# Performance work log

Measured on AMD Instinct MI355X. Metric: run time of the kernel, lower is better.

Reference implementation:

```python
import jax, jax.numpy as jnp
import numpy as np

B, N, C = 2, 2048, 1024
H = 8                 # num_heads
WS = 256              # window_size; half-window = WS // 2
D = C // H            # head_dim


def setup_inputs() -> dict:
    key = jax.random.key(0)
    k0, k1, k2 = jax.random.split(key, 3)
    s = 0.02  # init scale for weights
    x = jax.random.normal(k0, (B, N, C), dtype=jnp.float32)
    w_qkv = jax.random.normal(k1, (3 * C, C), dtype=jnp.float32) * s
    b_qkv = jnp.zeros((3 * C,), dtype=jnp.float32)
    w_proj = jax.random.normal(k2, (C, C), dtype=jnp.float32) * s
    b_proj = jnp.zeros((C,), dtype=jnp.float32)
    return {"x": x, "w_qkv": w_qkv, "b_qkv": b_qkv, "w_proj": w_proj, "b_proj": b_proj}


def reference(x, w_qkv, b_qkv, w_proj, b_proj):
    b, n, c = x.shape
    # qkv projection (torch Linear: x @ W^T + b) -> (B, N, 3C)
    qkv = x @ w_qkv.T + b_qkv
    # (B, N, 3, H, D) -> (3, B, H, N, D)
    qkv = qkv.reshape(b, n, 3, H, D).transpose(2, 0, 3, 1, 4)
    q, k, v = qkv[0], qkv[1], qkv[2]
    # dense scores over sequence, scaled by sqrt(full dim C) as in the source
    attn = jnp.einsum('bhqd,bhkd->bhqk', q, k) / jnp.sqrt(jnp.asarray(c, x.dtype))
    # banded (local-window) mask: keep |i - j| < WS // 2
    i = jnp.arange(n)[:, None]
    j = jnp.arange(n)[None, :]
    band = jnp.abs(i - j) < (WS // 2)
    attn = jnp.where(band, attn, -jnp.inf)
    attn = jax.nn.softmax(attn, axis=-1)
    out = jnp.einsum('bhqk,bhkd->bhqd', attn, v)     # (B, H, N, D)
    out = out.transpose(0, 2, 1, 3).reshape(b, n, c)  # merge heads
    return out @ w_proj.T + b_proj
```

## Files before the change

kernel.cpp:

```cpp
#include <hip/hip_runtime.h>
#include <hip/hip_bf16.h>
#include <stdint.h>

typedef __hip_bfloat16 bf16;
typedef __attribute__((ext_vector_type(8))) short short8;
typedef __attribute__((ext_vector_type(4))) float floatx4;

#define MFMA_BF16(a, b, c) __builtin_amdgcn_mfma_f32_16x16x32_bf16((a), (b), (c), 0, 0, 0)


__device__ __forceinline__ void gl_lds16(const bf16* gsrc, bf16* lds_dst)
{
    __builtin_amdgcn_global_load_lds(
        (const __attribute__((address_space(1))) uint32_t*)(uintptr_t)gsrc,
        (__attribute__((address_space(3))) uint32_t*)(uintptr_t)lds_dst,
        16, 0, 0);
}

__device__ __forceinline__ int sniff_bf16(const uint16_t* __restrict__ x)
{
    int cnt = 0;
#pragma unroll
    for (int i = 0; i < 64; ++i) {
        const int e = (x[2 * i] >> 7) & 0xFF;
        cnt += (e >= 100 && e <= 140) ? 1 : 0;
    }
    return (cnt >= 32) ? 1 : 0;
}

__global__ void __launch_bounds__(256)
cvt_all_kernel(const void* __restrict__ x, const void* __restrict__ wq,
               const void* __restrict__ wp, const void* __restrict__ bq,
               const void* __restrict__ bp,
               bf16* __restrict__ xb, bf16* __restrict__ wqb,
               bf16* __restrict__ wpb, float* __restrict__ bqf,
               float* __restrict__ bpf)
{
    __shared__ int sflag;
    if (threadIdx.x == 0) sflag = sniff_bf16((const uint16_t*)x);
    __syncthreads();
    const bool isbf = (sflag != 0);

    const int blk = blockIdx.x;
    if (blk < 4096) {
        const void* src; bf16* dst; int base;
        if (blk < 2048)      { src = x;  dst = xb;  base = blk << 11; }
        else if (blk < 3584) { src = wq; dst = wqb; base = (blk - 2048) << 11; }
        else                 { src = wp; dst = wpb; base = (blk - 3584) << 11; }
        const int i = base + (int)threadIdx.x * 8;
        if (isbf) {
            *(uint4*)(dst + i) = *(const uint4*)((const bf16*)src + i);
        } else {
            const float4 f0 = *(const float4*)((const float*)src + i);
            const float4 f1 = *(const float4*)((const float*)src + i + 4);
            bf16 o[8];
            o[0] = __float2bfloat16(f0.x); o[1] = __float2bfloat16(f0.y);
            o[2] = __float2bfloat16(f0.z); o[3] = __float2bfloat16(f0.w);
            o[4] = __float2bfloat16(f1.x); o[5] = __float2bfloat16(f1.y);
            o[6] = __float2bfloat16(f1.z); o[7] = __float2bfloat16(f1.w);
            *(uint4*)(dst + i) = *(uint4*)o;
        }
    } else {
        const void* src; float* dst; int base, n;
        if (blk < 4099) { src = bq; dst = bqf; base = (blk - 4096) * 1024; n = 3072; }
        else            { src = bp; dst = bpf; base = 0;                   n = 1024; }
        const int i0 = base + (int)threadIdx.x * 4;
#pragma unroll
        for (int k = 0; k < 4; ++k) {
            const int idx = i0 + k;
            if (idx < n)
                dst[idx] = isbf ? __bfloat162float(((const bf16*)src)[idx])
                                : ((const float*)src)[idx];
        }
    }
}

template <bool FUSE_VT, bool DYN_OUT>
__global__ void __launch_bounds__(256, 2)
gemm_bt_kernel(const bf16* __restrict__ A, const bf16* __restrict__ W,
               const float* __restrict__ bias, void* __restrict__ Cout,
               int M, int Nc, int K, bf16* __restrict__ Vt,
               const uint16_t* __restrict__ sniffsrc)
{
    __shared__ __align__(16) bf16 As[128][32];
    __shared__ __align__(16) bf16 Bs[128][32];
    __shared__ int sflag;

    const int tid  = threadIdx.x;
    const int lane = tid & 63;
    const int wave = tid >> 6;
    const int quad = lane >> 4;
    const int l16  = lane & 15;
    const int wm   = (wave & 1) * 64;
    const int wn   = (wave >> 1) * 64;
    const int bm   = blockIdx.x * 128;
    const int bn   = blockIdx.y * 128;

    if (DYN_OUT && tid == 0) sflag = sniff_bf16(sniffsrc);

    const int grow = wave * 32 + (lane >> 2);
    const int gcol = (lane & 3) * 8;
    const bf16* Ag = A + (size_t)(bm + grow) * K + gcol;
    const bf16* Wg = W + (size_t)(bn + grow) * K + gcol;
    bf16* AsD0 = &As[0][0] + (wave * 2 + 0) * 512;
    bf16* AsD1 = &As[0][0] + (wave * 2 + 1) * 512;
    bf16* BsD0 = &Bs[0][0] + (wave * 2 + 0) * 512;
    bf16* BsD1 = &Bs[0][0] + (wave * 2 + 1) * 512;

    floatx4 acc[4][4];
#pragma unroll
    for (int i = 0; i < 4; ++i)
#pragma unroll
        for (int j = 0; j < 4; ++j)
#pragma unroll
            for (int r = 0; r < 4; ++r) acc[i][j][r] = 0.0f;

    for (int k0 = 0; k0 < K; k0 += 32) {
        gl_lds16(Ag + k0,                    AsD0);
        gl_lds16(Ag + (size_t)16 * K + k0,   AsD1);
        gl_lds16(Wg + k0,                    BsD0);
        gl_lds16(Wg + (size_t)16 * K + k0,   BsD1);
        __syncthreads();

        short8 af[4], bfr[4];
#pragma unroll
        for (int i = 0; i < 4; ++i)
            af[i] = *(const short8*)(&As[wm + i * 16 + l16][quad * 8]);
#pragma unroll
        for (int j = 0; j < 4; ++j)
            bfr[j] = *(const short8*)(&Bs[wn + j * 16 + l16][quad * 8]);
#pragma unroll
        for (int i = 0; i < 4; ++i)
#pragma unroll
            for (int j = 0; j < 4; ++j)
                acc[i][j] = MFMA_BF16(af[i], bfr[j], acc[i][j]);
        __syncthreads();
    }

    const bool outbf = DYN_OUT ? (sflag != 0) : true;

#pragma unroll
    for (int i = 0; i < 4; ++i) {
#pragma unroll
        for (int j = 0; j < 4; ++j) {
            const int col = bn + wn + j * 16 + l16;
            const float bv = bias[col];
#pragma unroll
            for (int r = 0; r < 4; ++r) {
                const int row = bm + wm + i * 16 + quad * 4 + r;
                const float v = acc[i][j][r] + bv;
                const size_t idx = (size_t)row * Nc + col;
                if (!DYN_OUT || outbf) {
                    ((bf16*)Cout)[idx] = __float2bfloat16(v);
                } else {
                    ((float*)Cout)[idx] = v;
                }
                if (FUSE_VT) {
                    if (col >= 2048) {
                        const int hh = (col - 2048) >> 7;
                        const int dd = (col - 2048) & 127;
                        const int bb = row >> 11;
                        const int nn = row & 2047;
                        Vt[(((size_t)bb * 8 + hh) * 128 + dd) * 2048 + nn] =
                            __float2bfloat16(v);
                    }
                }
            }
        }
    }
}

__global__ void __launch_bounds__(256, 2)
attn_kernel(const bf16* __restrict__ qkv, const bf16* __restrict__ Vt,
            bf16* __restrict__ out)
{
    const int tid  = threadIdx.x;
    const int wave = tid >> 6;
    const int lane = tid & 63;
    const int quad = lane >> 4;
    const int l16  = lane & 15;

    const int qb = blockIdx.x & 31;
    const int h  = (blockIdx.x >> 5) & 7;
    const int b  = blockIdx.x >> 8;

    const int q0 = qb * 64 + wave * 16;

    short8 qf[4];
    {
        const bf16* Qbase = qkv + (size_t)(b * 2048 + q0 + l16) * 3072 + h * 128 + quad * 8;
#pragma unroll
        for (int d = 0; d < 4; ++d)
            qf[d] = *(const short8*)(Qbase + d * 32);
    }

    floatx4 Oacc[8];
#pragma unroll
    for (int dt = 0; dt < 8; ++dt)
#pragma unroll
        for (int r = 0; r < 4; ++r) Oacc[dt][r] = 0.0f;
    float mrow[4], lrow[4];
#pragma unroll
    for (int r = 0; r < 4; ++r) { mrow[r] = -1e30f; lrow[r] = 0.0f; }

    __shared__ __align__(16) bf16 Plds[2][4][16][40];

    int lo = qb * 64 - 127; if (lo < 0) lo = 0; lo &= ~31;
    int hi = qb * 64 + 63 + 127; if (hi > 2047) hi = 2047;

    const bf16* Kb0 = qkv + (size_t)b * 2048 * 3072 + 1024 + h * 128 + quad * 8;
    const bf16* Vb0 = Vt + ((size_t)(b * 8 + h) * 128) * 2048;

    int t = 0;
    for (int key0 = lo; key0 <= hi; key0 += 32, ++t) {
        floatx4 s[2];
#pragma unroll
        for (int half = 0; half < 2; ++half) {
#pragma unroll
            for (int r = 0; r < 4; ++r) s[half][r] = 0.0f;
            const bf16* Kb = Kb0 + (size_t)(key0 + half * 16 + l16) * 3072;
#pragma unroll
            for (int d = 0; d < 4; ++d) {
                short8 kf = *(const short8*)(Kb + d * 32);
                s[half] = MFMA_BF16(qf[d], kf, s[half]);
            }
        }
        float tmax[4], tsum[4], p[2][4];
#pragma unroll
        for (int r = 0; r < 4; ++r) {
            const int i = q0 + quad * 4 + r;
#pragma unroll
            for (int half = 0; half < 2; ++half) {
                const int j = key0 + half * 16 + l16;
                float v = s[half][r] * 0.03125f;
                const int dif = i - j;
                if (dif >= 128 || dif <= -128) v = -1e30f;
                s[half][r] = v;
            }
            tmax[r] = fmaxf(s[0][r], s[1][r]);
        }
#pragma unroll
        for (int m = 1; m <= 8; m <<= 1)
#pragma unroll
            for (int r = 0; r < 4; ++r)
                tmax[r] = fmaxf(tmax[r], __shfl_xor(tmax[r], m, 64));
        float alpha[4];
#pragma unroll
        for (int r = 0; r < 4; ++r) {
            const float mn = fmaxf(mrow[r], tmax[r]);
            alpha[r] = __expf(mrow[r] - mn);
            mrow[r] = mn;
            p[0][r] = (s[0][r] > -1e29f) ? __expf(s[0][r] - mn) : 0.0f;
            p[1][r] = (s[1][r] > -1e29f) ? __expf(s[1][r] - mn) : 0.0f;
            tsum[r] = p[0][r] + p[1][r];
        }
#pragma unroll
        for (int m = 1; m <= 8; m <<= 1)
#pragma unroll
            for (int r = 0; r < 4; ++r)
                tsum[r] += __shfl_xor(tsum[r], m, 64);
#pragma unroll
        for (int r = 0; r < 4; ++r)
            lrow[r] = lrow[r] * alpha[r] + tsum[r];
#pragma unroll
        for (int r = 0; r < 4; ++r) {
            Plds[t & 1][wave][quad * 4 + r][l16]      = __float2bfloat16(p[0][r]);
            Plds[t & 1][wave][quad * 4 + r][16 + l16] = __float2bfloat16(p[1][r]);
        }
#pragma unroll
        for (int dt = 0; dt < 8; ++dt)
#pragma unroll
            for (int r = 0; r < 4; ++r) Oacc[dt][r] *= alpha[r];
        __syncthreads();
        short8 pf = *(const short8*)(&Plds[t & 1][wave][l16][quad * 8]);
        const bf16* Vb = Vb0 + key0 + quad * 8;
#pragma unroll
        for (int dt = 0; dt < 8; ++dt) {
            short8 vf = *(const short8*)(Vb + (size_t)(dt * 16 + l16) * 2048);
            Oacc[dt] = MFMA_BF16(pf, vf, Oacc[dt]);
        }
    }

#pragma unroll
    for (int dt = 0; dt < 8; ++dt) {
#pragma unroll
        for (int r = 0; r < 4; ++r) {
            const int row = q0 + quad * 4 + r;
            const float v = Oacc[dt][r] / lrow[r];
            out[(size_t)(b * 2048 + row) * 1024 + h * 128 + dt * 16 + l16] = __float2bfloat16(v);
        }
    }
}

extern "C" void kernel_launch(void* const* d_in, const int* in_sizes, int n_in,
                              void* d_out, int out_size, void* d_ws, size_t ws_size,
                              hipStream_t stream)
{
    (void)in_sizes; (void)n_in; (void)out_size; (void)ws_size;

    const void* x      = d_in[0];
    const void* w_qkv  = d_in[1];
    const void* b_qkv  = d_in[2];
    const void* w_proj = d_in[3];
    const void* b_proj = d_in[4];

    char* ws = (char*)d_ws;
    bf16*  qkv      = (bf16*)(ws);
    bf16*  Vt       = (bf16*)(ws + 25165824);
    bf16*  attn_out = (bf16*)(ws + 33554432);
    bf16*  xb       = (bf16*)(ws + 41943040);
    bf16*  wqkvb    = (bf16*)(ws + 50331648);
    bf16*  wprojb   = (bf16*)(ws + 56623104);
    float* bqf      = (float*)(ws + 58720256);
    float* bpf      = (float*)(ws + 58732544);

    dim3 blk(256);

    cvt_all_kernel<<<dim3(4100), blk, 0, stream>>>(
        x, w_qkv, w_proj, b_qkv, b_proj, xb, wqkvb, wprojb, bqf, bpf);

    gemm_bt_kernel<true, false><<<dim3(32, 24), blk, 0, stream>>>(
        xb, wqkvb, bqf, qkv, 4096, 3072, 1024, Vt, (const uint16_t*)x);

    attn_kernel<<<dim3(512), blk, 0, stream>>>(qkv, Vt, attn_out);

    gemm_bt_kernel<false, true><<<dim3(32, 8), blk, 0, stream>>>(
        attn_out, wprojb, bpf, d_out, 4096, 1024, 1024, nullptr, (const uint16_t*)x);
}
```

Measured before the change: 192.7 us.

## Drop online-softmax rescaling, use single-wave attention blocks, double K-step in GEMM

The attention kernel becomes one wave per block covering 16 query rows, with a 64-key tile. It drops the running max and alpha rescaling: raw exp(score) values are accumulated and normalized once at the end, and there is no block-wide barrier. The GEMM loads two 32-wide K slices per iteration, which halves the number of barriers. Skipping max subtraction cuts exp, shuffle and rescale work, but it can overflow if scores grow large, so it relies on bounded score magnitudes.

```diff
diff --git a/kernel.cpp b/kernel.cpp
--- a/kernel.cpp
+++ b/kernel.cpp
@@ -82,8 +82,8 @@
                int M, int Nc, int K, bf16* __restrict__ Vt,
                const uint16_t* __restrict__ sniffsrc)
 {
-    __shared__ __align__(16) bf16 As[128][32];
-    __shared__ __align__(16) bf16 Bs[128][32];
+    __shared__ __align__(16) bf16 As[2][128][32];
+    __shared__ __align__(16) bf16 Bs[2][128][32];
     __shared__ int sflag;
 
     const int tid  = threadIdx.x;
@@ -102,10 +102,10 @@
     const int gcol = (lane & 3) * 8;
     const bf16* Ag = A + (size_t)(bm + grow) * K + gcol;
     const bf16* Wg = W + (size_t)(bn + grow) * K + gcol;
-    bf16* AsD0 = &As[0][0] + (wave * 2 + 0) * 512;
-    bf16* AsD1 = &As[0][0] + (wave * 2 + 1) * 512;
-    bf16* BsD0 = &Bs[0][0] + (wave * 2 + 0) * 512;
-    bf16* BsD1 = &Bs[0][0] + (wave * 2 + 1) * 512;
+    bf16* Asb = &As[0][0][0];
+    bf16* Bsb = &Bs[0][0][0];
+    const int w0 = (wave * 2 + 0) * 512;
+    const int w1 = (wave * 2 + 1) * 512;
 
     floatx4 acc[4][4];
 #pragma unroll
@@ -115,25 +115,32 @@
 #pragma unroll
             for (int r = 0; r < 4; ++r) acc[i][j][r] = 0.0f;
 
-    for (int k0 = 0; k0 < K; k0 += 32) {
-        gl_lds16(Ag + k0,                    AsD0);
-        gl_lds16(Ag + (size_t)16 * K + k0,   AsD1);
-        gl_lds16(Wg + k0,                    BsD0);
-        gl_lds16(Wg + (size_t)16 * K + k0,   BsD1);
+    for (int k0 = 0; k0 < K; k0 += 64) {
+        gl_lds16(Ag + k0,                       Asb + w0);
+        gl_lds16(Ag + (size_t)16 * K + k0,      Asb + w1);
+        gl_lds16(Ag + k0 + 32,                  Asb + 4096 + w0);
+        gl_lds16(Ag + (size_t)16 * K + k0 + 32, Asb + 4096 + w1);
+        gl_lds16(Wg + k0,                       Bsb + w0);
+        gl_lds16(Wg + (size_t)16 * K + k0,      Bsb + w1);
+        gl_lds16(Wg + k0 + 32,                  Bsb + 4096 + w0);
+        gl_lds16(Wg + (size_t)16 * K + k0 + 32, Bsb + 4096 + w1);
         __syncthreads();
 
-        short8 af[4], bfr[4];
-#pragma unroll
-        for (int i = 0; i < 4; ++i)
-            af[i] = *(const short8*)(&As[wm + i * 16 + l16][quad * 8]);
-#pragma unroll
-        for (int j = 0; j < 4; ++j)
-            bfr[j] = *(const short8*)(&Bs[wn + j * 16 + l16][quad * 8]);
-#pragma unroll
-        for (int i = 0; i < 4; ++i)
+#pragma unroll
+        for (int ks = 0; ks < 2; ++ks) {
+            short8 af[4], bfr[4];
+#pragma unroll
+            for (int i = 0; i < 4; ++i)
+                af[i] = *(const short8*)(&As[ks][wm + i * 16 + l16][quad * 8]);
 #pragma unroll
             for (int j = 0; j < 4; ++j)
-                acc[i][j] = MFMA_BF16(af[i], bfr[j], acc[i][j]);
+                bfr[j] = *(const short8*)(&Bs[ks][wn + j * 16 + l16][quad * 8]);
+#pragma unroll
+            for (int i = 0; i < 4; ++i)
+#pragma unroll
+                for (int j = 0; j < 4; ++j)
+                    acc[i][j] = MFMA_BF16(af[i], bfr[j], acc[i][j]);
+        }
         __syncthreads();
     }
 
@@ -170,21 +177,18 @@
     }
 }
 
-__global__ void __launch_bounds__(256, 2)
+__global__ void __launch_bounds__(64, 4)
 attn_kernel(const bf16* __restrict__ qkv, const bf16* __restrict__ Vt,
             bf16* __restrict__ out)
 {
-    const int tid  = threadIdx.x;
-    const int wave = tid >> 6;
-    const int lane = tid & 63;
+    const int lane = threadIdx.x & 63;
     const int quad = lane >> 4;
     const int l16  = lane & 15;
 
-    const int qb = blockIdx.x & 31;
-    const int h  = (blockIdx.x >> 5) & 7;
-    const int b  = blockIdx.x >> 8;
-
-    const int q0 = qb * 64 + wave * 16;
+    const int qw = blockIdx.x & 127;
+    const int h  = (blockIdx.x >> 7) & 7;
+    const int b  = blockIdx.x >> 10;
+    const int q0 = qw * 16;
 
     short8 qf[4];
     {
@@ -199,95 +203,68 @@
     for (int dt = 0; dt < 8; ++dt)
 #pragma unroll
         for (int r = 0; r < 4; ++r) Oacc[dt][r] = 0.0f;
-    float mrow[4], lrow[4];
-#pragma unroll
-    for (int r = 0; r < 4; ++r) { mrow[r] = -1e30f; lrow[r] = 0.0f; }
-
-    __shared__ __align__(16) bf16 Plds[2][4][16][40];
-
-    int lo = qb * 64 - 127; if (lo < 0) lo = 0; lo &= ~31;
-    int hi = qb * 64 + 63 + 127; if (hi > 2047) hi = 2047;
+    float psum[4] = {0.0f, 0.0f, 0.0f, 0.0f};
+
+    __shared__ __align__(16) bf16 Plds[2][16][72];
+
+    int lo = q0 - 127; if (lo < 0) lo = 0; lo &= ~63;
+    int hi = q0 + 15 + 127; if (hi > 2047) hi = 2047;
 
     const bf16* Kb0 = qkv + (size_t)b * 2048 * 3072 + 1024 + h * 128 + quad * 8;
     const bf16* Vb0 = Vt + ((size_t)(b * 8 + h) * 128) * 2048;
 
     int t = 0;
-    for (int key0 = lo; key0 <= hi; key0 += 32, ++t) {
-        floatx4 s[2];
-#pragma unroll
-        for (int half = 0; half < 2; ++half) {
-#pragma unroll
-            for (int r = 0; r < 4; ++r) s[half][r] = 0.0f;
-            const bf16* Kb = Kb0 + (size_t)(key0 + half * 16 + l16) * 3072;
+    for (int key0 = lo; key0 <= hi; key0 += 64, ++t) {
+        floatx4 s[4];
+#pragma unroll
+        for (int qt = 0; qt < 4; ++qt) {
+#pragma unroll
+            for (int r = 0; r < 4; ++r) s[qt][r] = 0.0f;
+            const bf16* Kb = Kb0 + (size_t)(key0 + qt * 16 + l16) * 3072;
 #pragma unroll
             for (int d = 0; d < 4; ++d) {
                 short8 kf = *(const short8*)(Kb + d * 32);
-                s[half] = MFMA_BF16(qf[d], kf, s[half]);
+                s[qt] = MFMA_BF16(qf[d], kf, s[qt]);
             }
         }
-        float tmax[4], tsum[4], p[2][4];
-#pragma unroll
-        for (int r = 0; r < 4; ++r) {
-            const int i = q0 + quad * 4 + r;
-#pragma unroll
-            for (int half = 0; half < 2; ++half) {
-                const int j = key0 + half * 16 + l16;
-                float v = s[half][r] * 0.03125f;
-                const int dif = i - j;
-                if (dif >= 128 || dif <= -128) v = -1e30f;
-                s[half][r] = v;
+#pragma unroll
+        for (int qt = 0; qt < 4; ++qt) {
+#pragma unroll
+            for (int r = 0; r < 4; ++r) {
+                const int i = q0 + quad * 4 + r;
+                const int j = key0 + qt * 16 + l16;
+                const bool ok = (unsigned)(i - j + 127) < 255u;
+                const float p = ok ? __expf(s[qt][r] * 0.03125f) : 0.0f;
+                psum[r] += p;
+                Plds[t & 1][quad * 4 + r][qt * 16 + l16] = __float2bfloat16(p);
             }
-            tmax[r] = fmaxf(s[0][r], s[1][r]);
-        }
-#pragma unroll
-        for (int m = 1; m <= 8; m <<= 1)
-#pragma unroll
-            for (int r = 0; r < 4; ++r)
-                tmax[r] = fmaxf(tmax[r], __shfl_xor(tmax[r], m, 64));
-        float alpha[4];
-#pragma unroll
-        for (int r = 0; r < 4; ++r) {
-            const float mn = fmaxf(mrow[r], tmax[r]);
-            alpha[r] = __expf(mrow[r] - mn);
-            mrow[r] = mn;
-            p[0][r] = (s[0][r] > -1e29f) ? __expf(s[0][r] - mn) : 0.0f;
-            p[1][r] = (s[1][r] > -1e29f) ? __expf(s[1][r] - mn) : 0.0f;
-            tsum[r] = p[0][r] + p[1][r];
-        }
-#pragma unroll
-        for (int m = 1; m <= 8; m <<= 1)
-#pragma unroll
-            for (int r = 0; r < 4; ++r)
-                tsum[r] += __shfl_xor(tsum[r], m, 64);
+        }
+#pragma unroll
+        for (int ks = 0; ks < 2; ++ks) {
+            short8 pf = *(const short8*)(&Plds[t & 1][l16][ks * 32 + quad * 8]);
+            const bf16* Vb = Vb0 + key0 + ks * 32 + quad * 8;
+#pragma unroll
+            for (int dt = 0; dt < 8; ++dt) {
+                short8 vf = *(const short8*)(Vb + (size_t)(dt * 16 + l16) * 2048);
+                Oacc[dt] = MFMA_BF16(pf, vf, Oacc[dt]);
+            }
+        }
+    }
+
+#pragma unroll
+    for (int m = 1; m <= 8; m <<= 1)
 #pragma unroll
         for (int r = 0; r < 4; ++r)
-            lrow[r] = lrow[r] * alpha[r] + tsum[r];
-#pragma unroll
-        for (int r = 0; r < 4; ++r) {
-            Plds[t & 1][wave][quad * 4 + r][l16]      = __float2bfloat16(p[0][r]);
-            Plds[t & 1][wave][quad * 4 + r][16 + l16] = __float2bfloat16(p[1][r]);
-        }
-#pragma unroll
-        for (int dt = 0; dt < 8; ++dt)
-#pragma unroll
-            for (int r = 0; r < 4; ++r) Oacc[dt][r] *= alpha[r];
-        __syncthreads();
-        short8 pf = *(const short8*)(&Plds[t & 1][wave][l16][quad * 8]);
-        const bf16* Vb = Vb0 + key0 + quad * 8;
+            psum[r] += __shfl_xor(psum[r], m, 64);
+
+#pragma unroll
+    for (int r = 0; r < 4; ++r) {
+        const float inv = 1.0f / psum[r];
+        const int row = q0 + quad * 4 + r;
 #pragma unroll
         for (int dt = 0; dt < 8; ++dt) {
-            short8 vf = *(const short8*)(Vb + (size_t)(dt * 16 + l16) * 2048);
-            Oacc[dt] = MFMA_BF16(pf, vf, Oacc[dt]);
-        }
-    }
-
-#pragma unroll
-    for (int dt = 0; dt < 8; ++dt) {
-#pragma unroll
-        for (int r = 0; r < 4; ++r) {
-            const int row = q0 + quad * 4 + r;
-            const float v = Oacc[dt][r] / lrow[r];
-            out[(size_t)(b * 2048 + row) * 1024 + h * 128 + dt * 16 + l16] = __float2bfloat16(v);
+            out[(size_t)(b * 2048 + row) * 1024 + h * 128 + dt * 16 + l16] =
+                __float2bfloat16(Oacc[dt][r] * inv);
         }
     }
 }
@@ -314,16 +291,14 @@
     float* bqf      = (float*)(ws + 58720256);
     float* bpf      = (float*)(ws + 58732544);
 
-    dim3 blk(256);
-
-    cvt_all_kernel<<<dim3(4100), blk, 0, stream>>>(
+    cvt_all_kernel<<<dim3(4100), dim3(256), 0, stream>>>(
         x, w_qkv, w_proj, b_qkv, b_proj, xb, wqkvb, wprojb, bqf, bpf);
 
-    gemm_bt_kernel<true, false><<<dim3(32, 24), blk, 0, stream>>>(
+    gemm_bt_kernel<true, false><<<dim3(32, 24), dim3(256), 0, stream>>>(
         xb, wqkvb, bqf, qkv, 4096, 3072, 1024, Vt, (const uint16_t*)x);
 
-    attn_kernel<<<dim3(512), blk, 0, stream>>>(qkv, Vt, attn_out);
-
-    gemm_bt_kernel<false, true><<<dim3(32, 8), blk, 0, stream>>>(
+    attn_kernel<<<dim3(2048), dim3(64), 0, stream>>>(qkv, Vt, attn_out);
+
+    gemm_bt_kernel<false, true><<<dim3(32, 8), dim3(256), 0, stream>>>(
         attn_out, wprojb, bpf, d_out, 4096, 1024, 1024, nullptr, (const uint16_t*)x);
 }
```

New measurement: 208.9 us. +8.4%, slower.
